# Optimization experiments

Measured on AMD Instinct MI355X. Metric: run time of the kernel, lower is better.

## Reference

```python
import jax, jax.numpy as jnp
import numpy as np

B, S, E, H = 4, 1024, 1024, 16
D = E // H  # head dim = 64

def setup_inputs() -> dict:
    key = jax.random.key(0)
    k1, k2, k3, k4, k5 = jax.random.split(key, 5)
    return {
        "lstm_out": jax.random.normal(k1, (B, S, E), dtype=jnp.float32),
        "in_proj_weight": jax.random.normal(k2, (3 * E, E), dtype=jnp.float32) * 0.02,
        "in_proj_bias": jax.random.normal(k3, (3 * E,), dtype=jnp.float32) * 0.02,
        "out_proj_weight": jax.random.normal(k4, (E, E), dtype=jnp.float32) * 0.02,
        "out_proj_bias": jax.random.normal(k5, (E,), dtype=jnp.float32) * 0.02,
    }

def reference(lstm_out, in_proj_weight, in_proj_bias, out_proj_weight, out_proj_bias):
    # Packed QKV projection, as in nn.MultiheadAttention (Linear uses x @ W.T + b)
    qkv = lstm_out @ in_proj_weight.T + in_proj_bias          # [B,S,3E]
    q, k, v = jnp.split(qkv, 3, axis=-1)                      # each [B,S,E]
    def heads(t):
        return t.reshape(B, S, H, D).transpose(0, 2, 1, 3)    # [B,H,S,D]
    q, k, v = heads(q), heads(k), heads(v)
    scale = 1.0 / jnp.sqrt(jnp.asarray(D, dtype=q.dtype))
    scores = jnp.einsum("bhsd,bhtd->bhst", q * scale, k)      # [B,H,S,S]
    attn = jax.nn.softmax(scores, axis=-1)                    # [B,H,S,S]
    ctx = jnp.einsum("bhst,bhtd->bhsd", attn, v)              # [B,H,S,D]
    ctx = ctx.transpose(0, 2, 1, 3).reshape(B, S, E)          # [B,S,E]
    attn_output = ctx @ out_proj_weight.T + out_proj_bias     # [B,S,E]
    # need_weights=True with default average_attn_weights=True -> mean over heads
    attn_weights = attn.mean(axis=1)                          # [B,S,S]
    context_vector = attn_output.mean(axis=1)                 # [B,E]
    return (context_vector, attn_weights)
```

## Files before the change

kernel.cpp:

```cpp
#include <hip/hip_runtime.h>


typedef unsigned short u16;
using s16x8 = __attribute__((ext_vector_type(8))) short;
using f32x4 = __attribute__((ext_vector_type(4))) float;
using u16x4 = __attribute__((ext_vector_type(4))) unsigned short;

#define AS1 __attribute__((address_space(1)))
#define AS3 __attribute__((address_space(3)))

#define QSCALE 0.1803368801111204f

__device__ __forceinline__ u16 f2bf(float f) {
    unsigned u = __float_as_uint(f);
    u += 0x7fffu + ((u >> 16) & 1u);
    return (u16)(u >> 16);
}

__global__ void k_prep(const float* __restrict__ X, const float* __restrict__ W1,
                       u16* __restrict__ Xb, u16* __restrict__ W1b,
                       float* __restrict__ cmean) {
    int i = blockIdx.x * blockDim.x + threadIdx.x;
    const float* src; u16* dst; int off;
    if (i < 1048576)       { src = X;  dst = Xb;  off = i; }
    else                   { src = W1; dst = W1b; off = i - 1048576; }
    float4 v = reinterpret_cast<const float4*>(src)[off];
    u16x4 o = { f2bf(v.x), f2bf(v.y), f2bf(v.z), f2bf(v.w) };
    reinterpret_cast<u16x4*>(dst)[off] = o;
    if (i < 4096) cmean[i] = 0.f;
}

__global__ __launch_bounds__(512) void k_gemm_bt(
    const u16* __restrict__ A, const u16* __restrict__ B,
    const float* __restrict__ bias, u16* __restrict__ C,
    u16* __restrict__ vt) {
    const int K = 1024;
    const int nbx = gridDim.x;
    const int nwg = nbx * gridDim.y;
    const int bid = blockIdx.y * nbx + blockIdx.x;
    const int per = nwg >> 3;
    const int swz = (bid & 7) * per + (bid >> 3);
    const int n0 = (swz % nbx) * 128, m0 = (swz / nbx) * 128;
    const int tid = threadIdx.x, lane = tid & 63, w = tid >> 6;
    const int wm = w >> 1, wn = w & 1;
    const int g = lane >> 4, l15 = lane & 15;
    __shared__ __attribute__((aligned(16))) u16 As[2][128 * 64];
    __shared__ __attribute__((aligned(16))) u16 Bs[2][128 * 64];

    f32x4 acc[2][4];
    #pragma unroll
    for (int mi = 0; mi < 2; ++mi)
        #pragma unroll
        for (int nj = 0; nj < 4; ++nj) acc[mi][nj] = (f32x4){0.f, 0.f, 0.f, 0.f};

    auto STAGE = [&](int k0, int sb) {
        #pragma unroll
        for (int r = 0; r < 2; ++r) {
            int c = tid + r * 512;
            int row = c >> 3, j = c & 7;
            int js = j ^ (row & 7);
            __builtin_amdgcn_global_load_lds(
                (AS1 const void*)(A + (size_t)(m0 + row) * K + k0 + js * 8),
                (AS3 void*)(&As[sb][c * 8]), 16, 0, 0);
            __builtin_amdgcn_global_load_lds(
                (AS1 const void*)(B + (size_t)(n0 + row) * K + k0 + js * 8),
                (AS3 void*)(&Bs[sb][c * 8]), 16, 0, 0);
        }
    };

    STAGE(0, 0);
    int buf = 0;
    for (int k0 = 0; k0 < K; k0 += 64) {
        __syncthreads();
        if (k0 + 64 < K) STAGE(k0 + 64, buf ^ 1);
        #pragma unroll
        for (int kk = 0; kk < 64; kk += 32) {
            const int cx0 = (((kk >> 3) + g) ^ (l15 & 7)) * 8;
            s16x8 av[2], bv[4];
            #pragma unroll
            for (int mi = 0; mi < 2; ++mi)
                av[mi] = *reinterpret_cast<const s16x8*>(
                    &As[buf][(wm * 32 + mi * 16 + l15) * 64 + cx0]);
            #pragma unroll
            for (int nj = 0; nj < 4; ++nj)
                bv[nj] = *reinterpret_cast<const s16x8*>(
                    &Bs[buf][(wn * 64 + nj * 16 + l15) * 64 + cx0]);
            #pragma unroll
            for (int mi = 0; mi < 2; ++mi)
                #pragma unroll
                for (int nj = 0; nj < 4; ++nj)
                    acc[mi][nj] = __builtin_amdgcn_mfma_f32_16x16x32_bf16(av[mi], bv[nj], acc[mi][nj], 0, 0, 0);
        }
        buf ^= 1;
    }

    #pragma unroll
    for (int nj = 0; nj < 4; ++nj) {
        int n = n0 + wn * 64 + nj * 16 + l15;
        float scale = (n < 1024) ? QSCALE : 1.0f;
        float bvs = bias[n] * scale;
        if (n < 2048) {
            #pragma unroll
            for (int mi = 0; mi < 2; ++mi)
                #pragma unroll
                for (int i = 0; i < 4; ++i) {
                    int m = m0 + wm * 32 + mi * 16 + g * 4 + i;
                    C[(size_t)m * 2048 + n] = f2bf(acc[mi][nj][i] * scale + bvs);
                }
        } else {
            int hd = n - 2048;
            #pragma unroll
            for (int mi = 0; mi < 2; ++mi)
                #pragma unroll
                for (int i = 0; i < 4; ++i) {
                    int m = m0 + wm * 32 + mi * 16 + g * 4 + i;
                    int b = m >> 10, t = m & 1023;
                    vt[((size_t)(b * 16 + (hd >> 6)) * 64 + (hd & 63)) * 1024 + t] =
                        f2bf(acc[mi][nj][i] + bvs);
                }
        }
    }
}

__global__ __launch_bounds__(512, 2) void k_flash(const u16* __restrict__ qk,
                                                  const u16* __restrict__ vt,
                                                  float* __restrict__ ml,
                                                  float* __restrict__ cmean) {
    const int id = blockIdx.x + 8 * (blockIdx.y + 16 * blockIdx.z);
    const int x = id & 7, k = id >> 3;
    const int gbh = x * 8 + (k >> 3);
    const int qt = k & 7;
    const int b = gbh >> 4, h = gbh & 15;
    const int q0 = qt * 128;
    const int tid = threadIdx.x, lane = tid & 63, w = tid >> 6;
    const int g = lane >> 4, l15 = lane & 15;
    __shared__ __attribute__((aligned(16))) u16 Ks[2][64 * 64];
    __shared__ __attribute__((aligned(16))) u16 Vt[3][64 * 64];
    __shared__ __attribute__((aligned(16))) u16 Ps[8][16 * 64];

    const size_t rowQ = (size_t)(b * 1024 + q0 + w * 16 + l15) * 2048 + h * 64;
    const s16x8 qa0 = *reinterpret_cast<const s16x8*>(qk + rowQ + g * 8);
    const s16x8 qa1 = *reinterpret_cast<const s16x8*>(qk + rowQ + 32 + g * 8);
    const s16x8 onesv = { (short)0x3F80, (short)0x3F80, (short)0x3F80, (short)0x3F80,
                          (short)0x3F80, (short)0x3F80, (short)0x3F80, (short)0x3F80 };

    const int rowA = tid >> 3, jA = tid & 7;
    const int dKA = tid * 8;
    const u16* kbase0 = qk + (size_t)(b * 1024) * 2048 + 1024 + h * 64;
    const u16* vtb = vt + (size_t)(b * 16 + h) * 65536;
    const u16* gKA = kbase0 + (size_t)rowA * 2048 + ((jA ^ (rowA & 7)) * 8);
    const u16* gVA = vtb + (size_t)rowA * 1024 + ((jA ^ (rowA & 7)) * 8);

    int kO[2][4], vO[2], pO[2], pW[4];
    #pragma unroll
    for (int tj = 0; tj < 4; ++tj) {
        int trow = tj * 16 + l15;
        kO[0][tj] = trow * 64 + ((g ^ (trow & 7)) * 8);
        kO[1][tj] = trow * 64 + (((4 + g) ^ (trow & 7)) * 8);
        pW[tj] = l15 * 64 + (((tj * 2 + (g >> 1)) ^ (l15 & 7)) * 8) + (g & 1) * 4;
    }
    pO[0] = l15 * 64 + ((g ^ (l15 & 7)) * 8);
    pO[1] = l15 * 64 + (((4 + g) ^ (l15 & 7)) * 8);
    vO[0] = pO[0];
    vO[1] = pO[1];

    f32x4 ctxa[4];
    #pragma unroll
    for (int nj = 0; nj < 4; ++nj) ctxa[nj] = (f32x4){0.f, 0.f, 0.f, 0.f};
    f32x4 lacc = (f32x4){0.f, 0.f, 0.f, 0.f};

    auto QK = [&](const u16* Kb, f32x4* sc) {
        #pragma unroll
        for (int tj = 0; tj < 4; ++tj) sc[tj] = (f32x4){0.f, 0.f, 0.f, 0.f};
        __builtin_amdgcn_s_setprio(1);
        #pragma unroll
        for (int kki = 0; kki < 2; ++kki) {
            s16x8 qa = kki ? qa1 : qa0;
            #pragma unroll
            for (int tj = 0; tj < 4; ++tj) {
                s16x8 kb = *reinterpret_cast<const s16x8*>(Kb + kO[kki][tj]);
                sc[tj] = __builtin_amdgcn_mfma_f32_16x16x32_bf16(kb, qa, sc[tj], 0, 0, 0);
            }
        }
        __builtin_amdgcn_s_setprio(0);
    };
    auto SMPV = [&](f32x4* sc, const u16* Vb) {
        #pragma unroll
        for (int tj = 0; tj < 4; ++tj)
            #pragma unroll
            for (int i = 0; i < 4; ++i)
                sc[tj][i] = exp2f(sc[tj][i]);
        u16* Pw = &Ps[w][0];
        #pragma unroll
        for (int tj = 0; tj < 4; ++tj) {
            unsigned pk01, pk23;
            asm("v_cvt_pk_bf16_f32 %0, %1, %2" : "=v"(pk01) : "v"(sc[tj][0]), "v"(sc[tj][1]));
            asm("v_cvt_pk_bf16_f32 %0, %1, %2" : "=v"(pk23) : "v"(sc[tj][2]), "v"(sc[tj][3]));
            uint2 pk = { pk01, pk23 };
            *reinterpret_cast<uint2*>(Pw + pW[tj]) = pk;
        }
        __builtin_amdgcn_s_setprio(1);
        #pragma unroll
        for (int kki = 0; kki < 2; ++kki) {
            s16x8 pa = *reinterpret_cast<const s16x8*>(Pw + pO[kki]);
            lacc = __builtin_amdgcn_mfma_f32_16x16x32_bf16(pa, onesv, lacc, 0, 0, 0);
            #pragma unroll
            for (int nj = 0; nj < 4; ++nj) {
                s16x8 vb = *reinterpret_cast<const s16x8*>(Vb + nj * 1024 + vO[kki]);
                ctxa[nj] = __builtin_amdgcn_mfma_f32_16x16x32_bf16(pa, vb, ctxa[nj], 0, 0, 0);
            }
        }
        __builtin_amdgcn_s_setprio(0);
    };

    __builtin_amdgcn_global_load_lds((AS1 const void*)gKA, (AS3 void*)(&Ks[0][dKA]), 16, 0, 0);
    __builtin_amdgcn_global_load_lds((AS1 const void*)gVA, (AS3 void*)(&Vt[0][dKA]), 16, 0, 0);
    gKA += 64 * 2048; gVA += 64;

    f32x4 scP[4];
    __syncthreads();
    __builtin_amdgcn_global_load_lds((AS1 const void*)gKA, (AS3 void*)(&Ks[1][dKA]), 16, 0, 0);
    __builtin_amdgcn_global_load_lds((AS1 const void*)gVA, (AS3 void*)(&Vt[1][dKA]), 16, 0, 0);
    gKA += 64 * 2048; gVA += 64;
    QK(&Ks[0][0], scP);

    #pragma unroll
    for (int kt = 1; kt < 16; ++kt) {
        __syncthreads();
        if (kt < 15) {
            __builtin_amdgcn_global_load_lds((AS1 const void*)gKA,
                (AS3 void*)(&Ks[(kt + 1) & 1][dKA]), 16, 0, 0);
            __builtin_amdgcn_global_load_lds((AS1 const void*)gVA,
                (AS3 void*)(&Vt[(kt + 1) % 3][dKA]), 16, 0, 0);
            gKA += 64 * 2048; gVA += 64;
        }
        f32x4 scC[4];
        QK(&Ks[kt & 1][0], scC);
        SMPV(scP, &Vt[(kt - 1) % 3][0]);
        #pragma unroll
        for (int tj = 0; tj < 4; ++tj) scP[tj] = scC[tj];
    }
    SMPV(scP, &Vt[15 % 3][0]);

    float inv_i[4];
    #pragma unroll
    for (int i = 0; i < 4; ++i) {
        inv_i[i] = 1.0f / lacc[i];
        if (l15 == 0)
            ml[(size_t)(b * 16 + h) * 1024 + q0 + w * 16 + g * 4 + i] = inv_i[i] * 0.0625f;
    }

    #pragma unroll
    for (int nj = 0; nj < 4; ++nj) {
        float s = ctxa[nj][0] * inv_i[0] + ctxa[nj][1] * inv_i[1]
                + ctxa[nj][2] * inv_i[2] + ctxa[nj][3] * inv_i[3];
        s += __shfl_xor(s, 16);
        s += __shfl_xor(s, 32);
        if (g == 0)
            atomicAdd(&cmean[b * 1024 + h * 64 + nj * 16 + l15], s * (1.0f / 1024.0f));
    }
}

__global__ __launch_bounds__(256, 4) void k_attnw(const u16* __restrict__ qk,
                                                  const float* __restrict__ ml,
                                                  float* __restrict__ attnw) {
    const int tt = blockIdx.x, stp = blockIdx.y, b = blockIdx.z;
    const int s0a = stp * 128, t0 = tt * 64;
    const int tid = threadIdx.x, lane = tid & 63, w = tid >> 6;
    const int g = lane >> 4, l15 = lane & 15;
    __shared__ __attribute__((aligned(16))) u16 Ks[2][64 * 64];
    __shared__ float mls[16][128];

    #pragma unroll
    for (int r = 0; r < 8; ++r) {
        int idx = tid + r * 256;
        int hh = idx >> 7, row = idx & 127;
        mls[hh][row] = ml[(size_t)(b * 16 + hh) * 1024 + s0a + row];
    }

    const int cA = tid, cB = tid + 256;
    const int rowA = cA >> 3, jA = cA & 7, rowB = cB >> 3, jB = cB & 7;
    const u16* kbase = qk + (size_t)(b * 1024 + t0) * 2048 + 1024;
    const size_t rowQa = (size_t)(b * 1024 + s0a + w * 16 + l15) * 2048;
    const size_t rowQb = rowQa + (size_t)64 * 2048;

    __builtin_amdgcn_global_load_lds((AS1 const void*)(kbase + (size_t)rowA * 2048 + ((jA ^ (rowA & 7)) * 8)),
                                     (AS3 void*)(&Ks[0][cA * 8]), 16, 0, 0);
    __builtin_amdgcn_global_load_lds((AS1 const void*)(kbase + (size_t)rowB * 2048 + ((jB ^ (rowB & 7)) * 8)),
                                     (AS3 void*)(&Ks[0][cB * 8]), 16, 0, 0);
    s16x8 qcA0 = *reinterpret_cast<const s16x8*>(qk + rowQa + g * 8);
    s16x8 qcA1 = *reinterpret_cast<const s16x8*>(qk + rowQa + 32 + g * 8);
    s16x8 qcB0 = *reinterpret_cast<const s16x8*>(qk + rowQb + g * 8);
    s16x8 qcB1 = *reinterpret_cast<const s16x8*>(qk + rowQb + 32 + g * 8);

    f32x4 accA[4], accB[4];
    #pragma unroll
    for (int tj = 0; tj < 4; ++tj) {
        accA[tj] = (f32x4){0.f, 0.f, 0.f, 0.f};
        accB[tj] = (f32x4){0.f, 0.f, 0.f, 0.f};
    }

    int buf = 0;
    for (int h = 0; h < 16; ++h) {
        __syncthreads();
        s16x8 qnA0, qnA1, qnB0, qnB1;
        if (h < 15) {
            const u16* kb2 = kbase + (h + 1) * 64;
            __builtin_amdgcn_global_load_lds((AS1 const void*)(kb2 + (size_t)rowA * 2048 + ((jA ^ (rowA & 7)) * 8)),
                                             (AS3 void*)(&Ks[buf ^ 1][cA * 8]), 16, 0, 0);
            __builtin_amdgcn_global_load_lds((AS1 const void*)(kb2 + (size_t)rowB * 2048 + ((jB ^ (rowB & 7)) * 8)),
                                             (AS3 void*)(&Ks[buf ^ 1][cB * 8]), 16, 0, 0);
            qnA0 = *reinterpret_cast<const s16x8*>(qk + rowQa + (h + 1) * 64 + g * 8);
            qnA1 = *reinterpret_cast<const s16x8*>(qk + rowQa + (h + 1) * 64 + 32 + g * 8);
            qnB0 = *reinterpret_cast<const s16x8*>(qk + rowQb + (h + 1) * 64 + g * 8);
            qnB1 = *reinterpret_cast<const s16x8*>(qk + rowQb + (h + 1) * 64 + 32 + g * 8);
        }

        f32x4 scA[4], scB[4];
        #pragma unroll
        for (int tj = 0; tj < 4; ++tj) {
            scA[tj] = (f32x4){0.f, 0.f, 0.f, 0.f};
            scB[tj] = (f32x4){0.f, 0.f, 0.f, 0.f};
        }
        #pragma unroll
        for (int kk = 0; kk < 64; kk += 32) {
            s16x8 qaA = kk ? qcA1 : qcA0;
            s16x8 qaB = kk ? qcB1 : qcB0;
            #pragma unroll
            for (int tj = 0; tj < 4; ++tj) {
                int trow = tj * 16 + l15;
                s16x8 kb = *reinterpret_cast<const s16x8*>(
                    &Ks[buf][trow * 64 + ((((kk >> 3) + g) ^ (trow & 7)) * 8)]);
                scA[tj] = __builtin_amdgcn_mfma_f32_16x16x32_bf16(qaA, kb, scA[tj], 0, 0, 0);
                scB[tj] = __builtin_amdgcn_mfma_f32_16x16x32_bf16(qaB, kb, scB[tj], 0, 0, 0);
            }
        }
        #pragma unroll
        for (int i = 0; i < 4; ++i) {
            int row = w * 16 + g * 4 + i;
            float Ma = mls[h][row];
            float Mb = mls[h][64 + row];
            #pragma unroll
            for (int tj = 0; tj < 4; ++tj) {
                accA[tj][i] += exp2f(scA[tj][i]) * Ma;
                accB[tj][i] += exp2f(scB[tj][i]) * Mb;
            }
        }
        qcA0 = qnA0; qcA1 = qnA1; qcB0 = qnB0; qcB1 = qnB1;
        buf ^= 1;
    }

    #pragma unroll
    for (int i = 0; i < 4; ++i) {
        int rowa = s0a + w * 16 + g * 4 + i;
        #pragma unroll
        for (int tj = 0; tj < 4; ++tj) {
            attnw[(size_t)(b * 1024 + rowa) * 1024 + t0 + tj * 16 + l15] = accA[tj][i];
            attnw[(size_t)(b * 1024 + rowa + 64) * 1024 + t0 + tj * 16 + l15] = accB[tj][i];
        }
    }
}

__global__ __launch_bounds__(256) void k_outproj(const float* __restrict__ cmean,
                                                 const float* __restrict__ wout,
                                                 const float* __restrict__ bias,
                                                 float* __restrict__ out) {
    __shared__ float cs[4096];
    #pragma unroll
    for (int r = 0; r < 16; ++r) {
        int idx = threadIdx.x + r * 256;
        cs[idx] = cmean[idx];
    }
    __syncthreads();
    int G = blockIdx.x * 256 + threadIdx.x;
    int e = G >> 6, ls = G & 63;
    const float4* wr = reinterpret_cast<const float4*>(wout) + (size_t)e * 256 + ls * 4;
    const float4* c0 = reinterpret_cast<const float4*>(&cs[0]) + ls * 4;
    const float4* c1 = reinterpret_cast<const float4*>(&cs[1024]) + ls * 4;
    const float4* c2 = reinterpret_cast<const float4*>(&cs[2048]) + ls * 4;
    const float4* c3 = reinterpret_cast<const float4*>(&cs[3072]) + ls * 4;
    float s0 = 0.f, s1 = 0.f, s2 = 0.f, s3 = 0.f;
    #pragma unroll
    for (int k = 0; k < 4; ++k) {
        float4 wv = wr[k];
        float4 a = c0[k], b = c1[k], c = c2[k], d = c3[k];
        s0 += a.x * wv.x + a.y * wv.y + a.z * wv.z + a.w * wv.w;
        s1 += b.x * wv.x + b.y * wv.y + b.z * wv.z + b.w * wv.w;
        s2 += c.x * wv.x + c.y * wv.y + c.z * wv.z + c.w * wv.w;
        s3 += d.x * wv.x + d.y * wv.y + d.z * wv.z + d.w * wv.w;
    }
    #pragma unroll
    for (int off = 1; off < 64; off <<= 1) {
        s0 += __shfl_xor(s0, off);
        s1 += __shfl_xor(s1, off);
        s2 += __shfl_xor(s2, off);
        s3 += __shfl_xor(s3, off);
    }
    if (ls == 0) {
        float bv = bias[e];
        out[e]        = s0 + bv;
        out[1024 + e] = s1 + bv;
        out[2048 + e] = s2 + bv;
        out[3072 + e] = s3 + bv;
    }
}

extern "C" void kernel_launch(void* const* d_in, const int* in_sizes, int n_in,
                              void* d_out, int out_size, void* d_ws, size_t ws_size,
                              hipStream_t stream) {
    const float* lstm = (const float*)d_in[0];
    const float* wqkv = (const float*)d_in[1];
    const float* bqkv = (const float*)d_in[2];
    const float* wout = (const float*)d_in[3];
    const float* bout = (const float*)d_in[4];
    float* out = (float*)d_out;

    char* ws = (char*)d_ws;
    u16*   Xbf   = (u16*)(ws);
    u16*   Wqkvb = (u16*)(ws + 8u  * 1024 * 1024);
    u16*   qkbuf = (u16*)(ws + 16u * 1024 * 1024);
    u16*   vtg   = (u16*)(ws + 32u * 1024 * 1024);
    float* ml    = (float*)(ws + 40u * 1024 * 1024);
    float* cmean = (float*)(ws + 41u * 1024 * 1024);

    k_prep<<<7168, 256, 0, stream>>>(lstm, wqkv, Xbf, Wqkvb, cmean);

    k_gemm_bt<<<dim3(24, 32), 512, 0, stream>>>(Xbf, Wqkvb, bqkv, qkbuf, vtg);
    k_flash<<<dim3(8, 16, 4), 512, 0, stream>>>(qkbuf, vtg, ml, cmean);
    k_attnw<<<dim3(16, 8, 4), 256, 0, stream>>>(qkbuf, ml, out + 4096);
    k_outproj<<<256, 256, 0, stream>>>(cmean, wout, bout, out);
}
```

Before: 114.0 us.

## Software-pipeline QK MFMA with exp2 finalize in attention-weights kernel

Restructures the per-head loop in k_attnw so the QK^T MFMAs for head h run alongside the exp2/scale accumulation for head h-1. It also fully unrolls the head loop, precomputes the swizzled LDS offsets, and raises MFMA issue priority with s_setprio. Occupancy is lowered from 4 to 3 blocks per SIMD in launch bounds to make room for the extra live score registers. The aim is to hide transcendental and VALU latency behind matrix work, at the cost of higher register pressure and lower occupancy.

New measurement: 258.1 us. 126% more time.

```diff
diff --git a/kernel.cpp b/kernel.cpp
--- a/kernel.cpp
+++ b/kernel.cpp
@@ -261,7 +261,7 @@
     }
 }
 
-__global__ __launch_bounds__(256, 4) void k_attnw(const u16* __restrict__ qk,
+__global__ __launch_bounds__(256, 3) void k_attnw(const u16* __restrict__ qk,
                                                   const float* __restrict__ ml,
                                                   float* __restrict__ attnw) {
     const int tt = blockIdx.x, stp = blockIdx.y, b = blockIdx.z;
@@ -284,71 +284,98 @@
     const size_t rowQa = (size_t)(b * 1024 + s0a + w * 16 + l15) * 2048;
     const size_t rowQb = rowQa + (size_t)64 * 2048;
 
-    __builtin_amdgcn_global_load_lds((AS1 const void*)(kbase + (size_t)rowA * 2048 + ((jA ^ (rowA & 7)) * 8)),
-                                     (AS3 void*)(&Ks[0][cA * 8]), 16, 0, 0);
-    __builtin_amdgcn_global_load_lds((AS1 const void*)(kbase + (size_t)rowB * 2048 + ((jB ^ (rowB & 7)) * 8)),
-                                     (AS3 void*)(&Ks[0][cB * 8]), 16, 0, 0);
+    int kO[2][4];
+    #pragma unroll
+    for (int tj = 0; tj < 4; ++tj) {
+        int trow = tj * 16 + l15;
+        kO[0][tj] = trow * 64 + ((g ^ (trow & 7)) * 8);
+        kO[1][tj] = trow * 64 + (((4 + g) ^ (trow & 7)) * 8);
+    }
+
+    auto KSTAGE = [&](int h, int sb) {
+        const u16* kb2 = kbase + h * 64;
+        __builtin_amdgcn_global_load_lds((AS1 const void*)(kb2 + (size_t)rowA * 2048 + ((jA ^ (rowA & 7)) * 8)),
+                                         (AS3 void*)(&Ks[sb][cA * 8]), 16, 0, 0);
+        __builtin_amdgcn_global_load_lds((AS1 const void*)(kb2 + (size_t)rowB * 2048 + ((jB ^ (rowB & 7)) * 8)),
+                                         (AS3 void*)(&Ks[sb][cB * 8]), 16, 0, 0);
+    };
+
+    f32x4 accA[4], accB[4];
+    #pragma unroll
+    for (int tj = 0; tj < 4; ++tj) {
+        accA[tj] = (f32x4){0.f, 0.f, 0.f, 0.f};
+        accB[tj] = (f32x4){0.f, 0.f, 0.f, 0.f};
+    }
+
+    KSTAGE(0, 0);
     s16x8 qcA0 = *reinterpret_cast<const s16x8*>(qk + rowQa + g * 8);
     s16x8 qcA1 = *reinterpret_cast<const s16x8*>(qk + rowQa + 32 + g * 8);
     s16x8 qcB0 = *reinterpret_cast<const s16x8*>(qk + rowQb + g * 8);
     s16x8 qcB1 = *reinterpret_cast<const s16x8*>(qk + rowQb + 32 + g * 8);
 
-    f32x4 accA[4], accB[4];
-    #pragma unroll
-    for (int tj = 0; tj < 4; ++tj) {
-        accA[tj] = (f32x4){0.f, 0.f, 0.f, 0.f};
-        accB[tj] = (f32x4){0.f, 0.f, 0.f, 0.f};
-    }
-
-    int buf = 0;
-    for (int h = 0; h < 16; ++h) {
+    auto QK2 = [&](const u16* Kb, s16x8 qA0, s16x8 qA1, s16x8 qB0, s16x8 qB1,
+                   f32x4* sA, f32x4* sB) {
+        #pragma unroll
+        for (int tj = 0; tj < 4; ++tj) {
+            sA[tj] = (f32x4){0.f, 0.f, 0.f, 0.f};
+            sB[tj] = (f32x4){0.f, 0.f, 0.f, 0.f};
+        }
+        __builtin_amdgcn_s_setprio(1);
+        #pragma unroll
+        for (int kki = 0; kki < 2; ++kki) {
+            s16x8 qa = kki ? qA1 : qA0;
+            s16x8 qb = kki ? qB1 : qB0;
+            #pragma unroll
+            for (int tj = 0; tj < 4; ++tj) {
+                s16x8 kb = *reinterpret_cast<const s16x8*>(Kb + kO[kki][tj]);
+                sA[tj] = __builtin_amdgcn_mfma_f32_16x16x32_bf16(qa, kb, sA[tj], 0, 0, 0);
+                sB[tj] = __builtin_amdgcn_mfma_f32_16x16x32_bf16(qb, kb, sB[tj], 0, 0, 0);
+            }
+        }
+        __builtin_amdgcn_s_setprio(0);
+    };
+    auto FIN = [&](int h, f32x4* sA, f32x4* sB) {
+        #pragma unroll
+        for (int i = 0; i < 4; ++i) {
+            int row = w * 16 + g * 4 + i;
+            float Ma = mls[h][row];
+            float Mb = mls[h][64 + row];
+            #pragma unroll
+            for (int tj = 0; tj < 4; ++tj) {
+                accA[tj][i] += exp2f(sA[tj][i]) * Ma;
+                accB[tj][i] += exp2f(sB[tj][i]) * Mb;
+            }
+        }
+    };
+
+    f32x4 scPA[4], scPB[4];
+    __syncthreads();
+    KSTAGE(1, 1);
+    s16x8 qnA0 = *reinterpret_cast<const s16x8*>(qk + rowQa + 64 + g * 8);
+    s16x8 qnA1 = *reinterpret_cast<const s16x8*>(qk + rowQa + 64 + 32 + g * 8);
+    s16x8 qnB0 = *reinterpret_cast<const s16x8*>(qk + rowQb + 64 + g * 8);
+    s16x8 qnB1 = *reinterpret_cast<const s16x8*>(qk + rowQb + 64 + 32 + g * 8);
+    QK2(&Ks[0][0], qcA0, qcA1, qcB0, qcB1, scPA, scPB);
+    qcA0 = qnA0; qcA1 = qnA1; qcB0 = qnB0; qcB1 = qnB1;
+
+    #pragma unroll
+    for (int h = 1; h < 16; ++h) {
         __syncthreads();
-        s16x8 qnA0, qnA1, qnB0, qnB1;
         if (h < 15) {
-            const u16* kb2 = kbase + (h + 1) * 64;
-            __builtin_amdgcn_global_load_lds((AS1 const void*)(kb2 + (size_t)rowA * 2048 + ((jA ^ (rowA & 7)) * 8)),
-                                             (AS3 void*)(&Ks[buf ^ 1][cA * 8]), 16, 0, 0);
-            __builtin_amdgcn_global_load_lds((AS1 const void*)(kb2 + (size_t)rowB * 2048 + ((jB ^ (rowB & 7)) * 8)),
-                                             (AS3 void*)(&Ks[buf ^ 1][cB * 8]), 16, 0, 0);
+            KSTAGE(h + 1, (h + 1) & 1);
             qnA0 = *reinterpret_cast<const s16x8*>(qk + rowQa + (h + 1) * 64 + g * 8);
             qnA1 = *reinterpret_cast<const s16x8*>(qk + rowQa + (h + 1) * 64 + 32 + g * 8);
             qnB0 = *reinterpret_cast<const s16x8*>(qk + rowQb + (h + 1) * 64 + g * 8);
             qnB1 = *reinterpret_cast<const s16x8*>(qk + rowQb + (h + 1) * 64 + 32 + g * 8);
         }
-
-        f32x4 scA[4], scB[4];
-        #pragma unroll
-        for (int tj = 0; tj < 4; ++tj) {
-            scA[tj] = (f32x4){0.f, 0.f, 0.f, 0.f};
-            scB[tj] = (f32x4){0.f, 0.f, 0.f, 0.f};
-        }
-        #pragma unroll
-        for (int kk = 0; kk < 64; kk += 32) {
-            s16x8 qaA = kk ? qcA1 : qcA0;
-            s16x8 qaB = kk ? qcB1 : qcB0;
-            #pragma unroll
-            for (int tj = 0; tj < 4; ++tj) {
-                int trow = tj * 16 + l15;
-                s16x8 kb = *reinterpret_cast<const s16x8*>(
-                    &Ks[buf][trow * 64 + ((((kk >> 3) + g) ^ (trow & 7)) * 8)]);
-                scA[tj] = __builtin_amdgcn_mfma_f32_16x16x32_bf16(qaA, kb, scA[tj], 0, 0, 0);
-                scB[tj] = __builtin_amdgcn_mfma_f32_16x16x32_bf16(qaB, kb, scB[tj], 0, 0, 0);
-            }
-        }
-        #pragma unroll
-        for (int i = 0; i < 4; ++i) {
-            int row = w * 16 + g * 4 + i;
-            float Ma = mls[h][row];
-            float Mb = mls[h][64 + row];
-            #pragma unroll
-            for (int tj = 0; tj < 4; ++tj) {
-                accA[tj][i] += exp2f(scA[tj][i]) * Ma;
-                accB[tj][i] += exp2f(scB[tj][i]) * Mb;
-            }
-        }
+        f32x4 scCA[4], scCB[4];
+        QK2(&Ks[h & 1][0], qcA0, qcA1, qcB0, qcB1, scCA, scCB);
+        FIN(h - 1, scPA, scPB);
+        #pragma unroll
+        for (int tj = 0; tj < 4; ++tj) { scPA[tj] = scCA[tj]; scPB[tj] = scCB[tj]; }
         qcA0 = qnA0; qcA1 = qnA1; qcB0 = qnB0; qcB1 = qnB1;
-        buf ^= 1;
-    }
+    }
+    FIN(15, scPA, scPB);
 
     #pragma unroll
     for (int i = 0; i < 4; ++i) {
```
